# Performance work log

Measured on AMD Instinct MI355X. Metric: run time of the kernel, lower is better.

Reference implementation:

```python
import jax, jax.numpy as jnp
import numpy as np


def setup_inputs() -> dict:
    key = jax.random.key(0)
    ks = jax.random.split(key, 8)
    B, L, U, D = 256, 16, 512, 2
    x = jax.random.randint(ks[0], (B, L, L), 0, D, dtype=jnp.int32)
    def s(k, shape, fan):
        return jax.random.normal(k, shape, jnp.float32) / np.float32(np.sqrt(fan))
    return {
        "x": x,
        "W_in_h": s(ks[1], (D, U), D),
        "W_in_v": s(ks[2], (D, U), D),
        "W_carry_h": s(ks[3], (U, U), U),
        "b_carry_h": jnp.zeros((U,), jnp.float32),
        "W_carry_v": s(ks[4], (U, U), U),
        "W_out": s(ks[5], (U, D), U),
        "b_out": jnp.zeros((D,), jnp.float32),
    }


def reference(x, W_in_h, W_in_v, W_carry_h, b_carry_h, W_carry_v, W_out, b_out):
    B, L = x.shape[0], x.shape[1]
    U = W_carry_h.shape[0]
    D = W_out.shape[1]

    # one-hot spins, padded: zero row above, zero columns left/right
    oh = jax.nn.one_hot(jnp.transpose(x, (1, 2, 0)), D, dtype=jnp.float32)  # (L,L,B,D)
    inputs = jnp.zeros((L + 1, L + 2, B, D), jnp.float32).at[1:, 1:-1].set(oh)
    direction = jnp.where(jnp.arange(L) % 2 == 0, 1, -1)  # boustrophedon row flips

    def rev(line, d):
        return jnp.where(d == 1, line, jnp.flip(line, 0))

    def cell(h, xs):
        xh, xv, cv = xs  # left one-hot (B,D), above one-hot (B,D), above hidden (B,U)
        new = jax.nn.elu(xh @ W_in_h + xv @ W_in_v + h @ W_carry_h + b_carry_h + cv @ W_carry_v)
        p = jax.nn.softmax(new @ W_out + b_out)  # (B,D)
        return new, (new, p)

    def row(states, xs):
        cur, prev, d = xs  # (L+2,B,D), (L+2,B,D), scalar direction
        cur_r, prev_r, st_r = rev(cur, d), rev(prev, d), rev(states, d)
        _, (new_states, probs) = jax.lax.scan(
            cell, jnp.zeros((B, U), jnp.float32),
            (cur_r[:-2], prev_r[1:-1], st_r))
        logp = jnp.log(jnp.sum(probs * cur_r[1:-1], axis=2))  # (L,B)
        return rev(new_states, d), jnp.sum(logp, axis=0)

    _, prob = jax.lax.scan(row, jnp.zeros((L, B, U), jnp.float32),
                           (inputs[1:], inputs[:-1], direction))
    return jnp.nan_to_num(jnp.sum(prob, axis=0))  # (B,) log-probabilities
```

## Files before the change

### kernel.cpp

```cpp
#include <hip/hip_runtime.h>
#include <hip/hip_bf16.h>
#include <math.h>

#define NT  512
#define NWG 128

typedef __attribute__((ext_vector_type(8))) short bf16x8;
typedef __attribute__((ext_vector_type(4))) float f32x4;

__device__ __forceinline__ unsigned short f2bf(float f) {
    union { __hip_bfloat16 h; unsigned short s; } u;
    u.h = __float2bfloat16(f);
    return u.s;
}
__device__ __forceinline__ float bf2f(unsigned short s) {
    union { float f; unsigned u; } v; v.u = ((unsigned)s) << 16; return v.f;
}
__device__ __forceinline__ int st_off(int row, int k) {
    return row * 512 + ((k & 504) ^ ((row & 7) << 3)) + (k & 7);
}
__device__ __forceinline__ void barL() {
    asm volatile("s_waitcnt lgkmcnt(0)" ::: "memory");
    __builtin_amdgcn_s_barrier();
}

__device__ __forceinline__ void mfma_a(f32x4& d, bf16x8 a, bf16x8 b) {
    asm("v_mfma_f32_16x16x32_bf16 %0, %1, %2, %0" : "+a"(d) : "v"(a), "a"(b));
}
__device__ __forceinline__ void mfma_v(f32x4& d, bf16x8 a, bf16x8 b) {
    asm("v_mfma_f32_16x16x32_bf16 %0, %1, %2, %0" : "+a"(d) : "v"(a), "v"(b));
}

__global__ void conv_frag(const float* __restrict__ Wa, const float* __restrict__ Wb,
                          unsigned int* __restrict__ outa, unsigned int* __restrict__ outb) {
    const int bid = blockIdx.x;
    const float* W    = (bid < 512) ? Wa : Wb;
    unsigned int* out = (bid < 512) ? outa : outb;
    const int tile = bid & 511;
    const int l    = threadIdx.x;
    const int kb = tile >> 5, ub = tile & 31;
    const int k0 = kb * 32 + (l >> 4) * 8;
    const int u  = ub * 16 + (l & 15);
    unsigned v[4];
    #pragma unroll
    for (int p = 0; p < 4; ++p) {
        unsigned lo = f2bf(W[(size_t)(k0 + 2 * p) * 512 + u]);
        unsigned hi = f2bf(W[(size_t)(k0 + 2 * p + 1) * 512 + u]);
        v[p] = lo | (hi << 16);
    }
    *(uint4*)(out + (size_t)(tile * 64 + l) * 4) = make_uint4(v[0], v[1], v[2], v[3]);
}

#define IMFMA(A, B, C) __builtin_amdgcn_mfma_f32_16x16x32_bf16((A), (B), (C), 0, 0, 0)

__global__ __launch_bounds__(NT)
__attribute__((amdgpu_waves_per_eu(2, 2)))
void rnn2d_v6(
    const int*   __restrict__ x,
    const float* __restrict__ Wih,
    const float* __restrict__ Wiv,
    const float* __restrict__ bch,
    const float* __restrict__ Wout,
    const float* __restrict__ bout,
    const unsigned int* __restrict__ wchf,
    const unsigned int* __restrict__ wcvf,
    float*       __restrict__ out)
{
    __shared__ __attribute__((aligned(16))) bf16x8        wlds[8 * 10 * 64];
    __shared__ __attribute__((aligned(16))) unsigned short stm[32 * 512];
    __shared__ __attribute__((aligned(16))) unsigned short Vb[32 * 512];
    __shared__ __attribute__((aligned(16))) unsigned short hb[2][2][512];
    __shared__ __attribute__((aligned(16))) float          part[512 * 2];
    __shared__ int    xc[2][2][16];
    __shared__ float4 wred[2][8];

    const int tid = threadIdx.x;
    const int b0  = blockIdx.x * 2;
    const int w   = tid >> 6, l = tid & 63;
    const int r   = l & 15,  hi4 = l >> 4, rb = r & 1;

    const float wih0 = Wih[tid], wih1 = Wih[512 + tid];
    const float wiv0 = Wiv[tid], wiv1 = Wiv[512 + tid];
    const float bc   = bch[tid];
    const float wo0  = Wout[2 * tid], wo1 = Wout[2 * tid + 1];
    const float bo0  = bout[0],       bo1 = bout[1];

    const bf16x8* __restrict__ WF = (const bf16x8*)wchf;
    const bf16x8* __restrict__ VF = (const bf16x8*)wcvf;

    for (int idx = tid; idx < 32 * 512 / 2; idx += NT) {
        ((unsigned*)stm)[idx] = 0;
        ((unsigned*)Vb)[idx]  = 0;
    }

    bf16x8 wregV[12];
    #pragma unroll
    for (int kb = 0; kb < 12; ++kb)
        wregV[kb] = WF[(kb * 32 + w * 4 + 0) * 64 + l];
    bf16x8 wagA[16];
    #pragma unroll
    for (int kb = 0; kb < 16; ++kb)
        wagA[kb] = WF[(kb * 32 + w * 4 + 1) * 64 + l];
    bf16x8 wagB[8];
    #pragma unroll
    for (int kb = 0; kb < 8; ++kb)
        wagB[kb] = WF[(kb * 32 + w * 4 + 2) * 64 + l];
    #pragma unroll
    for (int q = 0; q < 4; ++q)
        wlds[(w * 10 + q) * 64 + l] = WF[((12 + q) * 32 + w * 4 + 0) * 64 + l];
    #pragma unroll
    for (int q = 0; q < 6; ++q)
        wlds[(w * 10 + 4 + q) * 64 + l] = WF[((8 + q) * 32 + w * 4 + 2) * 64 + l];
    bf16x8 S[9];
    #pragma unroll
    for (int j = 0; j < 9; ++j)
        S[j] = WF[(j * 32 + w * 4 + 3) * 64 + l];

    float logp0 = 0.f, logp1 = 0.f;
    int p = 0;

    for (int i = 0; i < 16; ++i) {
        const int dir = (i & 1) ? -1 : 1;

        if (i > 0) {
            const int kl = hi4 * 8;
            #pragma unroll
            for (int half = 0; half < 2; ++half) {
                f32x4 vacc[2][2];
                #pragma unroll
                for (int m = 0; m < 2; ++m)
                    #pragma unroll
                    for (int t4 = 0; t4 < 2; ++t4) vacc[m][t4] = (f32x4)(0.f);
                for (int kb = 0; kb < 16; ++kb) {
                    const int ka = kb * 32 + kl;
                    bf16x8 A0 = *(const bf16x8*)&stm[st_off(r,      ka)];
                    bf16x8 A1 = *(const bf16x8*)&stm[st_off(r + 16, ka)];
                    #pragma unroll
                    for (int t4 = 0; t4 < 2; ++t4) {
                        bf16x8 Bf = VF[(size_t)(kb * 32 + w * 4 + half * 2 + t4) * 64 + l];
                        vacc[0][t4] = IMFMA(A0, Bf, vacc[0][t4]);
                        vacc[1][t4] = IMFMA(A1, Bf, vacc[1][t4]);
                    }
                }
                #pragma unroll
                for (int m = 0; m < 2; ++m)
                    #pragma unroll
                    for (int t4 = 0; t4 < 2; ++t4)
                        #pragma unroll
                        for (int q = 0; q < 4; ++q)
                            Vb[(m * 16 + hi4 * 4 + q) * 512 +
                               (w * 4 + half * 2 + t4) * 16 + r] = f2bf(vacc[m][t4][q]);
            }
            #pragma unroll
            for (int j = 0; j < 9; ++j)
                S[j] = WF[(j * 32 + w * 4 + 3) * 64 + l];
        }

        if (tid < 64) {
            const int b = tid >> 5, rs = (tid >> 4) & 1, c = tid & 15;
            int v = 0;
            if (rs == 0)      v = x[(b0 + b) * 256 + i * 16 + c];
            else if (i > 0)   v = x[(b0 + b) * 256 + (i - 1) * 16 + c];
            xc[b][rs][c] = v;
        }
        ((unsigned*)hb)[tid] = 0;
        __syncthreads();

        for (int t = 0; t < 16; ++t) {
            const int c = (dir == 1) ? t : 15 - t;

            f32x4 acc0 = (f32x4)(0.f), acc1 = (f32x4)(0.f),
                  acc2 = (f32x4)(0.f), acc3 = (f32x4)(0.f);

            #define AF(KB) (*(const bf16x8*)&hb[p][rb][(((KB) * 4 + hi4) ^ rb) << 3])

            #pragma unroll
            for (int kb = 0; kb < 9; ++kb) {
                bf16x8 af = AF(kb);
                mfma_v(acc3, af, S[kb]);
                mfma_a(acc1, af, wagA[kb]);
                if (kb < 8) mfma_a(acc2, af, wagB[kb]);
                else        mfma_v(acc2, af, wlds[(w * 10 + 4) * 64 + l]);
                mfma_v(acc0, af, wregV[kb]);
            }
            #pragma unroll
            for (int j = 0; j < 7; ++j)
                S[j] = WF[((9 + j) * 32 + w * 4 + 3) * 64 + l];
            S[7] = WF[(14 * 32 + w * 4 + 2) * 64 + l];
            S[8] = WF[(15 * 32 + w * 4 + 2) * 64 + l];
            #pragma unroll
            for (int kb = 9; kb < 16; ++kb) {
                bf16x8 af = AF(kb);
                mfma_a(acc1, af, wagA[kb]);
                if (kb <= 11) mfma_v(acc0, af, wregV[kb]);
                else          mfma_v(acc0, af, wlds[(w * 10 + (kb - 12)) * 64 + l]);
                if (kb <= 13) mfma_v(acc2, af, wlds[(w * 10 + 4 + (kb - 8)) * 64 + l]);
                else          mfma_v(acc2, af, S[7 + (kb - 14)]);
                mfma_v(acc3, af, S[kb - 9]);
            }
            if (t < 15) {
                #pragma unroll
                for (int j = 0; j < 9; ++j)
                    S[j] = WF[(j * 32 + w * 4 + 3) * 64 + l];
            }
            #undef AF

            if (l < 16) {
                *(float2*)&part[(w * 64 +  0 + l) * 2] = make_float2(acc0[0], acc0[1]);
                *(float2*)&part[(w * 64 + 16 + l) * 2] = make_float2(acc1[0], acc1[1]);
                *(float2*)&part[(w * 64 + 32 + l) * 2] = make_float2(acc2[0], acc2[1]);
                *(float2*)&part[(w * 64 + 48 + l) * 2] = make_float2(acc3[0], acc3[1]);
            }
            barL();

            const int  cl   = c - dir;
            const bool hasL = (t > 0);
            const bool hasV = (i > 0);
            const float2 pa = *(const float2*)&part[tid * 2];
            float v0 = pa.x + bf2f(Vb[(c * 2 + 0) * 512 + tid]) + bc;
            float v1 = pa.y + bf2f(Vb[(c * 2 + 1) * 512 + tid]) + bc;
            if (hasL) { v0 += xc[0][0][cl] ? wih1 : wih0;  v1 += xc[1][0][cl] ? wih1 : wih0; }
            if (hasV) { v0 += xc[0][1][c]  ? wiv1 : wiv0;  v1 += xc[1][1][c]  ? wiv1 : wiv0; }
            v0 = v0 > 0.f ? v0 : expm1f(v0);
            v1 = v1 > 0.f ? v1 : expm1f(v1);
            hb[p ^ 1][0][(((tid >> 3) ^ 0) << 3) | (tid & 7)] = f2bf(v0);
            hb[p ^ 1][1][(((tid >> 3) ^ 1) << 3) | (tid & 7)] = f2bf(v1);
            stm[st_off(c * 2 + 0, tid)] = f2bf(v0);
            stm[st_off(c * 2 + 1, tid)] = f2bf(v1);
            const int sc0 = xc[0][0][c], sc1 = xc[1][0][c];
            float lp0 = v0 * wo0, lp1 = v0 * wo1, lp2 = v1 * wo0, lp3 = v1 * wo1;
            #pragma unroll
            for (int off = 32; off; off >>= 1) {
                lp0 += __shfl_down(lp0, off);
                lp1 += __shfl_down(lp1, off);
                lp2 += __shfl_down(lp2, off);
                lp3 += __shfl_down(lp3, off);
            }
            if (l == 0) wred[t & 1][w] = make_float4(lp0, lp1, lp2, lp3);
            barL();

            float g00 = bo0, g01 = bo1, g10 = bo0, g11 = bo1;
            #pragma unroll
            for (int ww = 0; ww < 8; ++ww) {
                const float4 v4 = wred[t & 1][ww];
                g00 += v4.x;  g01 += v4.y;  g10 += v4.z;  g11 += v4.w;
            }
            {
                const float m0 = fmaxf(g00, g01), m1 = fmaxf(g10, g11);
                const float ls0 = m0 + log1pf(expf(fminf(g00, g01) - m0));
                const float ls1 = m1 + log1pf(expf(fminf(g10, g11) - m1));
                logp0 += (sc0 ? g01 : g00) - ls0;
                logp1 += (sc1 ? g11 : g10) - ls1;
            }
            p ^= 1;
        }
    }

    if (tid < 2) {
        float v = tid ? logp1 : logp0;
        if (isnan(v)) v = 0.f;
        else if (isinf(v)) v = v > 0.f ? 3.4028235e38f : -3.4028235e38f;
        out[b0 + tid] = v;
    }
}

extern "C" void kernel_launch(void* const* d_in, const int* in_sizes, int n_in,
                              void* d_out, int out_size, void* d_ws, size_t ws_size,
                              hipStream_t stream) {
    const int*   x    = (const int*)  d_in[0];
    const float* Wih  = (const float*)d_in[1];
    const float* Wiv  = (const float*)d_in[2];
    const float* Wch  = (const float*)d_in[3];
    const float* bch  = (const float*)d_in[4];
    const float* Wcv  = (const float*)d_in[5];
    const float* Wout = (const float*)d_in[6];
    const float* bout = (const float*)d_in[7];

    unsigned int* ws_wch = (unsigned int*)d_ws;
    unsigned int* ws_wcv = (unsigned int*)((char*)d_ws + 512 * 1024);

    conv_frag<<<1024, 64, 0, stream>>>(Wch, Wcv, ws_wch, ws_wcv);
    rnn2d_v6<<<NWG, NT, 0, stream>>>(x, Wih, Wiv, bch, Wout, bout,
                                     ws_wch, ws_wcv, (float*)d_out);
}
```

Measured before the change: 2.513 ms.

## Repartition W_carry_h fragments across registers, LDS and double-buffered global streaming

Result: faster. 2.181 ms (-13.2%).

```diff
diff --git a/kernel.cpp b/kernel.cpp
--- a/kernel.cpp
+++ b/kernel.cpp
@@ -55,7 +55,7 @@
 
 __global__ __launch_bounds__(NT)
 __attribute__((amdgpu_waves_per_eu(2, 2)))
-void rnn2d_v6(
+void rnn2d_v7(
     const int*   __restrict__ x,
     const float* __restrict__ Wih,
     const float* __restrict__ Wiv,
@@ -78,6 +78,7 @@
     const int b0  = blockIdx.x * 2;
     const int w   = tid >> 6, l = tid & 63;
     const int r   = l & 15,  hi4 = l >> 4, rb = r & 1;
+    const int w4  = w * 4;
 
     const float wih0 = Wih[tid], wih1 = Wih[512 + tid];
     const float wiv0 = Wiv[tid], wiv1 = Wiv[512 + tid];
@@ -93,28 +94,36 @@
         ((unsigned*)Vb)[idx]  = 0;
     }
 
-    bf16x8 wregV[12];
-    #pragma unroll
-    for (int kb = 0; kb < 12; ++kb)
-        wregV[kb] = WF[(kb * 32 + w * 4 + 0) * 64 + l];
-    bf16x8 wagA[16];
+    bf16x8 wag0[16];
     #pragma unroll
     for (int kb = 0; kb < 16; ++kb)
-        wagA[kb] = WF[(kb * 32 + w * 4 + 1) * 64 + l];
-    bf16x8 wagB[8];
+        wag0[kb] = WF[(kb * 32 + w4 + 0) * 64 + l];
+    bf16x8 wag1[8];
     #pragma unroll
     for (int kb = 0; kb < 8; ++kb)
-        wagB[kb] = WF[(kb * 32 + w * 4 + 2) * 64 + l];
-    #pragma unroll
-    for (int q = 0; q < 4; ++q)
-        wlds[(w * 10 + q) * 64 + l] = WF[((12 + q) * 32 + w * 4 + 0) * 64 + l];
-    #pragma unroll
-    for (int q = 0; q < 6; ++q)
-        wlds[(w * 10 + 4 + q) * 64 + l] = WF[((8 + q) * 32 + w * 4 + 2) * 64 + l];
-    bf16x8 S[9];
-    #pragma unroll
-    for (int j = 0; j < 9; ++j)
-        S[j] = WF[(j * 32 + w * 4 + 3) * 64 + l];
+        wag1[kb] = WF[(kb * 32 + w4 + 1) * 64 + l];
+    #pragma unroll
+    for (int q = 0; q < 8; ++q)
+        wlds[(w * 10 + q) * 64 + l] = WF[((8 + q) * 32 + w4 + 1) * 64 + l];
+    #pragma unroll
+    for (int q = 0; q < 2; ++q)
+        wlds[(w * 10 + 8 + q) * 64 + l] = WF[(q * 32 + w4 + 2) * 64 + l];
+
+    bf16x8 SA[6], SB[6];
+    #define LOAD_PH0(B_) { _Pragma("unroll") for (int j = 0; j < 6; ++j) \
+        (B_)[j] = WF[((2 + j) * 32 + w4 + 2) * 64 + l]; }
+    #define LOAD_PH1(B_) { _Pragma("unroll") for (int j = 0; j < 6; ++j) \
+        (B_)[j] = WF[((8 + j) * 32 + w4 + 2) * 64 + l]; }
+    #define LOAD_PH2(B_) { _Pragma("unroll") for (int j = 0; j < 2; ++j) \
+        (B_)[j] = WF[((14 + j) * 32 + w4 + 2) * 64 + l]; \
+        _Pragma("unroll") for (int j = 2; j < 6; ++j) \
+        (B_)[j] = WF[((j - 2) * 32 + w4 + 3) * 64 + l]; }
+    #define LOAD_PH3(B_) { _Pragma("unroll") for (int j = 0; j < 6; ++j) \
+        (B_)[j] = WF[((4 + j) * 32 + w4 + 3) * 64 + l]; }
+    #define LOAD_PH4(B_) { _Pragma("unroll") for (int j = 0; j < 6; ++j) \
+        (B_)[j] = WF[((10 + j) * 32 + w4 + 3) * 64 + l]; }
+
+    LOAD_PH0(SA);
 
     float logp0 = 0.f, logp1 = 0.f;
     int p = 0;
@@ -137,7 +146,7 @@
                     bf16x8 A1 = *(const bf16x8*)&stm[st_off(r + 16, ka)];
                     #pragma unroll
                     for (int t4 = 0; t4 < 2; ++t4) {
-                        bf16x8 Bf = VF[(size_t)(kb * 32 + w * 4 + half * 2 + t4) * 64 + l];
+                        bf16x8 Bf = VF[(size_t)(kb * 32 + w4 + half * 2 + t4) * 64 + l];
                         vacc[0][t4] = IMFMA(A0, Bf, vacc[0][t4]);
                         vacc[1][t4] = IMFMA(A1, Bf, vacc[1][t4]);
                     }
@@ -149,11 +158,9 @@
                         #pragma unroll
                         for (int q = 0; q < 4; ++q)
                             Vb[(m * 16 + hi4 * 4 + q) * 512 +
-                               (w * 4 + half * 2 + t4) * 16 + r] = f2bf(vacc[m][t4][q]);
-            }
-            #pragma unroll
-            for (int j = 0; j < 9; ++j)
-                S[j] = WF[(j * 32 + w * 4 + 3) * 64 + l];
+                               (w4 + half * 2 + t4) * 16 + r] = f2bf(vacc[m][t4][q]);
+            }
+            LOAD_PH0(SA);
         }
 
         if (tid < 64) {
@@ -174,35 +181,36 @@
 
             #define AF(KB) (*(const bf16x8*)&hb[p][rb][(((KB) * 4 + hi4) ^ rb) << 3])
 
-            #pragma unroll
-            for (int kb = 0; kb < 9; ++kb) {
+            LOAD_PH1(SB);
+            #pragma unroll
+            for (int kb = 0; kb < 8; ++kb) {
                 bf16x8 af = AF(kb);
-                mfma_v(acc3, af, S[kb]);
-                mfma_a(acc1, af, wagA[kb]);
-                if (kb < 8) mfma_a(acc2, af, wagB[kb]);
-                else        mfma_v(acc2, af, wlds[(w * 10 + 4) * 64 + l]);
-                mfma_v(acc0, af, wregV[kb]);
-            }
-            #pragma unroll
-            for (int j = 0; j < 7; ++j)
-                S[j] = WF[((9 + j) * 32 + w * 4 + 3) * 64 + l];
-            S[7] = WF[(14 * 32 + w * 4 + 2) * 64 + l];
-            S[8] = WF[(15 * 32 + w * 4 + 2) * 64 + l];
-            #pragma unroll
-            for (int kb = 9; kb < 16; ++kb) {
+                mfma_a(acc0, af, wag0[kb]);
+                mfma_a(acc1, af, wag1[kb]);
+                if (kb < 2) mfma_v(acc2, af, wlds[(w * 10 + 8 + kb) * 64 + l]);
+            }
+            #pragma unroll
+            for (int j = 0; j < 6; ++j) { bf16x8 af = AF(2 + j); mfma_v(acc2, af, SA[j]); }
+            LOAD_PH2(SA);
+            #pragma unroll
+            for (int kb = 8; kb < 16; ++kb) {
                 bf16x8 af = AF(kb);
-                mfma_a(acc1, af, wagA[kb]);
-                if (kb <= 11) mfma_v(acc0, af, wregV[kb]);
-                else          mfma_v(acc0, af, wlds[(w * 10 + (kb - 12)) * 64 + l]);
-                if (kb <= 13) mfma_v(acc2, af, wlds[(w * 10 + 4 + (kb - 8)) * 64 + l]);
-                else          mfma_v(acc2, af, S[7 + (kb - 14)]);
-                mfma_v(acc3, af, S[kb - 9]);
-            }
-            if (t < 15) {
-                #pragma unroll
-                for (int j = 0; j < 9; ++j)
-                    S[j] = WF[(j * 32 + w * 4 + 3) * 64 + l];
-            }
+                mfma_a(acc0, af, wag0[kb]);
+                mfma_v(acc1, af, wlds[(w * 10 + kb - 8) * 64 + l]);
+            }
+            #pragma unroll
+            for (int j = 0; j < 6; ++j) { bf16x8 af = AF(8 + j); mfma_v(acc2, af, SB[j]); }
+            LOAD_PH3(SB);
+            #pragma unroll
+            for (int j = 0; j < 2; ++j) { bf16x8 af = AF(14 + j); mfma_v(acc2, af, SA[j]); }
+            #pragma unroll
+            for (int j = 2; j < 6; ++j) { bf16x8 af = AF(j - 2);  mfma_v(acc3, af, SA[j]); }
+            LOAD_PH4(SA);
+            #pragma unroll
+            for (int j = 0; j < 6; ++j) { bf16x8 af = AF(4 + j); mfma_v(acc3, af, SB[j]); }
+            #pragma unroll
+            for (int j = 0; j < 6; ++j) { bf16x8 af = AF(10 + j); mfma_v(acc3, af, SA[j]); }
+            if (t < 15) LOAD_PH0(SA);
             #undef AF
 
             if (l < 16) {
@@ -280,6 +288,6 @@
     unsigned int* ws_wcv = (unsigned int*)((char*)d_ws + 512 * 1024);
 
     conv_frag<<<1024, 64, 0, stream>>>(Wch, Wcv, ws_wch, ws_wcv);
-    rnn2d_v6<<<NWG, NT, 0, stream>>>(x, Wih, Wiv, bch, Wout, bout,
+    rnn2d_v7<<<NWG, NT, 0, stream>>>(x, Wih, Wiv, bch, Wout, bout,
                                      ws_wch, ws_wcv, (float*)d_out);
 }
```
